# Kernel optimization log

Measured on AMD Instinct MI355X. Metric: run time of the kernel, lower is better.

## Reference

```python
import jax, jax.numpy as jnp
import numpy as np

N, CIN, H, W = 32, 128, 56, 56
COUT, KH, KW = 256, 3, 3
PH, PW, SH, SW = 1, 1, 1, 1


def setup_inputs() -> dict:
    key = jax.random.key(0)
    kx, kw_, kb = jax.random.split(key, 3)
    x = jax.random.normal(kx, (N, CIN, H, W), dtype=jnp.float32)
    # kaiming_normal_ fan_in, relu: std = sqrt(2 / fan_in)
    fan_in = CIN * KH * KW
    weight = jax.random.normal(kw_, (COUT, CIN, KH, KW), dtype=jnp.float32) * jnp.sqrt(2.0 / fan_in)
    bias = jnp.zeros((COUT,), dtype=jnp.float32)
    return {"x": x, "weight": weight, "bias": bias}


def reference(x, weight, bias):
    # NCHW input, OIHW weight -> NCHW output; zero padding, stride (SH, SW)
    y = jax.lax.conv_general_dilated(
        x, weight,
        window_strides=(SH, SW),
        padding=((PH, PH), (PW, PW)),
        dimension_numbers=("NCHW", "OIHW", "NCHW"),
    )
    return y + bias[None, :, None, None]
```

## Files before the change

### kernel.cpp

```cpp
#include <hip/hip_runtime.h>
#include <hip/hip_bf16.h>


typedef __attribute__((ext_vector_type(8))) short bf16x8;
typedef __attribute__((ext_vector_type(4))) float f32x4;
typedef __attribute__((ext_vector_type(8))) unsigned short u16x8;

#define AS1(p) ((const __attribute__((address_space(1))) unsigned int*)(p))
#define AS3(p) ((__attribute__((address_space(3))) unsigned int*)(p))
#define G_LDS16(g, l) __builtin_amdgcn_global_load_lds(AS1(g), AS3(l), 16, 0, 0)

#define XT_OFF (1u << 20)

__global__ __launch_bounds__(256) void k_wreorder(const float* __restrict__ w,
                                                  __hip_bfloat16* __restrict__ wt) {
    int t = blockIdx.x * 256 + threadIdx.x;
    if (t >= 9 * 256 * 128) return;
    int ci = t & 127;
    int co = (t >> 7) & 255;
    int khkw = t >> 15;
    wt[t] = __float2bfloat16(w[(co * 128 + ci) * 9 + khkw]);
}

__global__ __launch_bounds__(256) void k_xconv(const float* __restrict__ x,
                                               __hip_bfloat16* __restrict__ xt) {
    const int b = blockIdx.x;
    const int n = b / 58, ih = b % 58;
    __hip_bfloat16* row = xt + (size_t)b * 58 * 128;
    const int t = threadIdx.x;

    if (ih == 0 || ih == 57) {
        u16x8 z = {0, 0, 0, 0, 0, 0, 0, 0};
        for (int i = t; i < 928; i += 256)
            ((u16x8*)row)[i] = z;
        return;
    }

    const int h = ih - 1;
    __shared__ float tile[56][132];
    const float* xb = x + (size_t)n * 128 * 3136 + h * 56;
    for (int i = t; i < 1792; i += 256) {
        int ci = i / 14, w4 = i % 14;
        f32x4 v = *(const f32x4*)(xb + ci * 3136 + w4 * 4);
#pragma unroll
        for (int c = 0; c < 4; ++c)
            tile[w4 * 4 + c][ci] = v[c];
    }
    __syncthreads();

    if (t < 32) {
        u16x8 z = {0, 0, 0, 0, 0, 0, 0, 0};
        int iw = (t < 16) ? 0 : 57;
        ((u16x8*)(row + iw * 128))[t & 15] = z;
    }
    for (int i = t; i < 896; i += 256) {
        int p = i >> 4, g = i & 15;
        u16x8 o;
#pragma unroll
        for (int j = 0; j < 8; ++j) {
            __hip_bfloat16 bv = __float2bfloat16(tile[p][g * 8 + j]);
            o[j] = *reinterpret_cast<unsigned short*>(&bv);
        }
        *(u16x8*)((char*)row + (p + 1) * 256 + g * 16) = o;
    }
}

__global__ __launch_bounds__(512, 2) void k_conv_gemm(
    const __hip_bfloat16* __restrict__ wt,
    const __hip_bfloat16* __restrict__ xt,
    const float* __restrict__ bias,
    float* __restrict__ out)
{
    __shared__ char lds[256 * 128 + 128 * 128];
    char* ldsA = lds;
    char* ldsB = lds + 256 * 128;

    const int bid = blockIdx.x;
    const int blk = (bid & 7) * 98 + (bid >> 3);

    const int tid = threadIdx.x;
    const int lane = tid & 63, wave = tid >> 6;
    const int co_w = (wave >> 1) * 64;
    const int px_w = (wave & 1) * 64;

    const int lr = lane >> 3;
    const int lc = lane & 7;
    const int swz = ((lc ^ lr) << 4);

    unsigned int bsrc[2];
#pragma unroll
    for (int r = 0; r < 2; ++r) {
        int px = r * 64 + wave * 8 + lr;
        int p = blk * 128 + px;
        int n = p / 3136, rem = p - n * 3136;
        int oh = rem / 56, ow = rem - oh * 56;
        bsrc[r] = (unsigned)(((n * 58 + oh) * 58 + ow) * 256) + swz;
    }

    f32x4 acc[4][4] = {};

    for (int khkw = 0; khkw < 9; ++khkw) {
        const int kh = khkw / 3, kw = khkw - kh * 3;
        const unsigned koffB = (unsigned)((kh * 58 + kw) * 256);
        const unsigned aoff = (unsigned)(khkw * 65536);
        for (int ci2 = 0; ci2 < 256; ci2 += 128) {
#pragma unroll
            for (int r = 0; r < 4; ++r) {
                int co = r * 64 + wave * 8 + lr;
                G_LDS16((const char*)wt + aoff + ci2 + co * 256 + swz,
                        ldsA + (r * 64 + wave * 8) * 128);
            }
#pragma unroll
            for (int r = 0; r < 2; ++r) {
                G_LDS16((const char*)xt + bsrc[r] + koffB + ci2,
                        ldsB + (r * 64 + wave * 8) * 128);
            }
            __syncthreads();

#pragma unroll
            for (int ks = 0; ks < 2; ++ks) {
                bf16x8 af[4], bx[4];
#pragma unroll
                for (int m = 0; m < 4; ++m) {
                    int row = co_w + m * 16 + (lane & 15);
                    int koff = (ks * 64 + ((lane >> 4) * 16)) ^ ((row & 7) << 4);
                    af[m] = *(const bf16x8*)(ldsA + row * 128 + koff);
                }
#pragma unroll
                for (int nn = 0; nn < 4; ++nn) {
                    int row = px_w + nn * 16 + (lane & 15);
                    int koff = (ks * 64 + ((lane >> 4) * 16)) ^ ((row & 7) << 4);
                    bx[nn] = *(const bf16x8*)(ldsB + row * 128 + koff);
                }
#pragma unroll
                for (int m = 0; m < 4; ++m)
#pragma unroll
                    for (int nn = 0; nn < 4; ++nn)
                        acc[m][nn] = __builtin_amdgcn_mfma_f32_16x16x32_bf16(
                            af[m], bx[nn], acc[m][nn], 0, 0, 0);
            }
            __syncthreads();
        }
    }

    int obase[4];
#pragma unroll
    for (int nn = 0; nn < 4; ++nn) {
        int p = blk * 128 + px_w + nn * 16 + (lane & 15);
        int n = p / 3136, rem = p - n * 3136;
        obase[nn] = n * 802816 + rem;
    }
    const int rgrp = lane >> 4;
#pragma unroll
    for (int m = 0; m < 4; ++m) {
#pragma unroll
        for (int r = 0; r < 4; ++r) {
            int co = co_w + m * 16 + rgrp * 4 + r;
            float bv = bias[co];
#pragma unroll
            for (int nn = 0; nn < 4; ++nn)
                out[obase[nn] + co * 3136] = acc[m][nn][r] + bv;
        }
    }
}

extern "C" void kernel_launch(void* const* d_in, const int* in_sizes, int n_in,
                              void* d_out, int out_size, void* d_ws, size_t ws_size,
                              hipStream_t stream) {
    const float* x    = (const float*)d_in[0];
    const float* w    = (const float*)d_in[1];
    const float* bias = (const float*)d_in[2];
    float* out = (float*)d_out;

    char* ws = (char*)d_ws;
    __hip_bfloat16* wt = (__hip_bfloat16*)ws;
    __hip_bfloat16* xt = (__hip_bfloat16*)(ws + XT_OFF);

    k_wreorder<<<1152, 256, 0, stream>>>(w, wt);
    k_xconv<<<32 * 58, 256, 0, stream>>>(x, xt);
    k_conv_gemm<<<784, 512, 0, stream>>>(wt, xt, bias, out);
}
```

Baseline: 206.5 us.

## Double-buffer input tile in LDS and read weights directly from global

Stops staging the weight tile through LDS. Each wave now loads its A fragments straight from global memory (served by L1/L2). The input tile B is double-buffered in LDS so the next step's async load overlaps the current MFMA work, and only one barrier remains per step instead of two. This cuts LDS footprint and synchronization, but the weight reads now go to global memory in the inner loop without reuse across waves sharing rows, which may expose memory latency.

```diff
diff --git a/kernel.cpp b/kernel.cpp
--- a/kernel.cpp
+++ b/kernel.cpp
@@ -71,9 +71,7 @@
     const float* __restrict__ bias,
     float* __restrict__ out)
 {
-    __shared__ char lds[256 * 128 + 128 * 128];
-    char* ldsA = lds;
-    char* ldsB = lds + 256 * 128;
+    __shared__ char ldsB[2][128 * 128];
 
     const int bid = blockIdx.x;
     const int blk = (bid & 7) * 98 + (bid >> 3);
@@ -97,50 +95,55 @@
         bsrc[r] = (unsigned)(((n * 58 + oh) * 58 + ow) * 256) + swz;
     }
 
+    const unsigned abase = (unsigned)((co_w + (lane & 15)) * 256 + (lane >> 4) * 16);
+
     f32x4 acc[4][4] = {};
 
-    for (int khkw = 0; khkw < 9; ++khkw) {
-        const int kh = khkw / 3, kw = khkw - kh * 3;
-        const unsigned koffB = (unsigned)((kh * 58 + kw) * 256);
-        const unsigned aoff = (unsigned)(khkw * 65536);
-        for (int ci2 = 0; ci2 < 256; ci2 += 128) {
+    {
 #pragma unroll
-            for (int r = 0; r < 4; ++r) {
-                int co = r * 64 + wave * 8 + lr;
-                G_LDS16((const char*)wt + aoff + ci2 + co * 256 + swz,
-                        ldsA + (r * 64 + wave * 8) * 128);
+        for (int r = 0; r < 2; ++r)
+            G_LDS16((const char*)xt + bsrc[r] +  0 +  0,
+                    ldsB[0] + (r * 64 + wave * 8) * 128);
+    }
+    __syncthreads();
+
+    int cur = 0;
+    for (int step = 0; step < 18; ++step) {
+        if (step + 1 < 18) {
+            int s = step + 1;
+            int kk = s >> 1, cih = s & 1;
+            int kh = kk / 3, kw = kk - kh * 3;
+            unsigned off = (unsigned)((kh * 58 + kw) * 256 + cih * 128);
+#pragma unroll
+            for (int r = 0; r < 2; ++r)
+                G_LDS16((const char*)xt + bsrc[r] + off,
+                        ldsB[cur ^ 1] + (r * 64 + wave * 8) * 128);
+        }
+
+        const int kk = step >> 1, cih = step & 1;
+        const unsigned aoff = (unsigned)(kk * 65536 + cih * 128) + abase;
+
+#pragma unroll
+        for (int khalf = 0; khalf < 2; ++khalf) {
+            bf16x8 af[4], bx[4];
+#pragma unroll
+            for (int m = 0; m < 4; ++m)
+                af[m] = *(const bf16x8*)((const char*)wt + aoff + m * 4096 + khalf * 64);
+#pragma unroll
+            for (int nn = 0; nn < 4; ++nn) {
+                int row = px_w + nn * 16 + (lane & 15);
+                int koff = (khalf * 64 + ((lane >> 4) * 16)) ^ ((row & 7) << 4);
+                bx[nn] = *(const bf16x8*)(ldsB[cur] + row * 128 + koff);
             }
 #pragma unroll
-            for (int r = 0; r < 2; ++r) {
-                G_LDS16((const char*)xt + bsrc[r] + koffB + ci2,
-                        ldsB + (r * 64 + wave * 8) * 128);
-            }
-            __syncthreads();
-
+            for (int m = 0; m < 4; ++m)
 #pragma unroll
-            for (int ks = 0; ks < 2; ++ks) {
-                bf16x8 af[4], bx[4];
-#pragma unroll
-                for (int m = 0; m < 4; ++m) {
-                    int row = co_w + m * 16 + (lane & 15);
-                    int koff = (ks * 64 + ((lane >> 4) * 16)) ^ ((row & 7) << 4);
-                    af[m] = *(const bf16x8*)(ldsA + row * 128 + koff);
-                }
-#pragma unroll
-                for (int nn = 0; nn < 4; ++nn) {
-                    int row = px_w + nn * 16 + (lane & 15);
-                    int koff = (ks * 64 + ((lane >> 4) * 16)) ^ ((row & 7) << 4);
-                    bx[nn] = *(const bf16x8*)(ldsB + row * 128 + koff);
-                }
-#pragma unroll
-                for (int m = 0; m < 4; ++m)
-#pragma unroll
-                    for (int nn = 0; nn < 4; ++nn)
-                        acc[m][nn] = __builtin_amdgcn_mfma_f32_16x16x32_bf16(
-                            af[m], bx[nn], acc[m][nn], 0, 0, 0);
-            }
-            __syncthreads();
+                for (int nn = 0; nn < 4; ++nn)
+                    acc[m][nn] = __builtin_amdgcn_mfma_f32_16x16x32_bf16(
+                        af[m], bx[nn], acc[m][nn], 0, 0, 0);
         }
+        __syncthreads();
+        cur ^= 1;
     }
 
     int obase[4];
```

Result: slower. 285.2 us (+38.1%).

## Triple-buffer LDS stages with async prefetch and one barrier per step

Applied to the files above, without the earlier changes.

The conv GEMM main loop now uses three LDS slots. Global-to-LDS loads for step t+2 are issued while step t computes, and partial vmcnt waits replace the two __syncthreads per iteration with a single barrier. MFMA issue is wrapped in s_setprio to favour math waves. LDS use rises to 144 KB per block, which may prevent two blocks per CU from fitting as the launch bounds request, trading occupancy for latency hiding.

```diff
diff --git a/kernel.cpp b/kernel.cpp
--- a/kernel.cpp
+++ b/kernel.cpp
@@ -71,17 +71,15 @@
     const float* __restrict__ bias,
     float* __restrict__ out)
 {
-    __shared__ char lds[256 * 128 + 128 * 128];
-    char* ldsA = lds;
-    char* ldsB = lds + 256 * 128;
+    __shared__ char lds[3][384 * 128];
 
     const int bid = blockIdx.x;
     const int blk = (bid & 7) * 98 + (bid >> 3);
 
     const int tid = threadIdx.x;
     const int lane = tid & 63, wave = tid >> 6;
-    const int co_w = (wave >> 1) * 64;
-    const int px_w = (wave & 1) * 64;
+    const int wm = wave >> 1;
+    const int wn = wave & 1;
 
     const int lr = lane >> 3;
     const int lc = lane & 7;
@@ -97,56 +95,76 @@
         bsrc[r] = (unsigned)(((n * 58 + oh) * 58 + ow) * 256) + swz;
     }
 
+    auto stage = [&](int s, char* slot) {
+        const int kk = s >> 1, cih = s & 1;
+        const int kh = kk / 3, kw = kk - kh * 3;
+        const unsigned aoff = (unsigned)(kk * 65536 + cih * 128);
+#pragma unroll
+        for (int r = 0; r < 4; ++r) {
+            int row = r * 64 + wave * 8;
+            G_LDS16((const char*)wt + aoff + (row + lr) * 256 + swz,
+                    slot + row * 128);
+        }
+        const unsigned boff = (unsigned)((kh * 58 + kw) * 256 + cih * 128);
+#pragma unroll
+        for (int r = 0; r < 2; ++r) {
+            G_LDS16((const char*)xt + bsrc[r] + boff,
+                    slot + (256 + r * 64 + wave * 8) * 128);
+        }
+    };
+
     f32x4 acc[4][4] = {};
 
-    for (int khkw = 0; khkw < 9; ++khkw) {
-        const int kh = khkw / 3, kw = khkw - kh * 3;
-        const unsigned koffB = (unsigned)((kh * 58 + kw) * 256);
-        const unsigned aoff = (unsigned)(khkw * 65536);
-        for (int ci2 = 0; ci2 < 256; ci2 += 128) {
-#pragma unroll
-            for (int r = 0; r < 4; ++r) {
-                int co = r * 64 + wave * 8 + lr;
-                G_LDS16((const char*)wt + aoff + ci2 + co * 256 + swz,
-                        ldsA + (r * 64 + wave * 8) * 128);
+    stage(0, lds[0]);
+    stage(1, lds[1]);
+
+    char* cs = lds[0];
+    char* ns = lds[1];
+    char* ps = lds[2];
+
+    for (int t = 0; t < 18; ++t) {
+        if (t < 17) asm volatile("s_waitcnt vmcnt(6)" ::: "memory");
+        else        asm volatile("s_waitcnt vmcnt(0)" ::: "memory");
+        __builtin_amdgcn_s_barrier();
+        __builtin_amdgcn_sched_barrier(0);
+
+        if (t < 16) stage(t + 2, ps);
+
+        bf16x8 af[2][4], bx[2][4];
+#pragma unroll
+        for (int kh2 = 0; kh2 < 2; ++kh2) {
+#pragma unroll
+            for (int m = 0; m < 4; ++m) {
+                int row = wm * 64 + m * 16 + (lane & 15);
+                int koff = (kh2 * 64 + ((lane >> 4) * 16)) ^ ((row & 7) << 4);
+                af[kh2][m] = *(const bf16x8*)(cs + row * 128 + koff);
             }
 #pragma unroll
-            for (int r = 0; r < 2; ++r) {
-                G_LDS16((const char*)xt + bsrc[r] + koffB + ci2,
-                        ldsB + (r * 64 + wave * 8) * 128);
+            for (int nn = 0; nn < 4; ++nn) {
+                int row = wn * 64 + nn * 16 + (lane & 15);
+                int koff = (kh2 * 64 + ((lane >> 4) * 16)) ^ ((row & 7) << 4);
+                bx[kh2][nn] = *(const bf16x8*)(cs + (256 + row) * 128 + koff);
             }
-            __syncthreads();
-
-#pragma unroll
-            for (int ks = 0; ks < 2; ++ks) {
-                bf16x8 af[4], bx[4];
-#pragma unroll
-                for (int m = 0; m < 4; ++m) {
-                    int row = co_w + m * 16 + (lane & 15);
-                    int koff = (ks * 64 + ((lane >> 4) * 16)) ^ ((row & 7) << 4);
-                    af[m] = *(const bf16x8*)(ldsA + row * 128 + koff);
-                }
-#pragma unroll
-                for (int nn = 0; nn < 4; ++nn) {
-                    int row = px_w + nn * 16 + (lane & 15);
-                    int koff = (ks * 64 + ((lane >> 4) * 16)) ^ ((row & 7) << 4);
-                    bx[nn] = *(const bf16x8*)(ldsB + row * 128 + koff);
-                }
-#pragma unroll
-                for (int m = 0; m < 4; ++m)
-#pragma unroll
-                    for (int nn = 0; nn < 4; ++nn)
-                        acc[m][nn] = __builtin_amdgcn_mfma_f32_16x16x32_bf16(
-                            af[m], bx[nn], acc[m][nn], 0, 0, 0);
-            }
-            __syncthreads();
-        }
+        }
+
+        __builtin_amdgcn_s_setprio(1);
+#pragma unroll
+        for (int kh2 = 0; kh2 < 2; ++kh2)
+#pragma unroll
+            for (int m = 0; m < 4; ++m)
+#pragma unroll
+                for (int nn = 0; nn < 4; ++nn)
+                    acc[m][nn] = __builtin_amdgcn_mfma_f32_16x16x32_bf16(
+                        af[kh2][m], bx[kh2][nn], acc[m][nn], 0, 0, 0);
+        __builtin_amdgcn_s_setprio(0);
+
+        char* tmp = cs; cs = ns; ns = ps; ps = tmp;
     }
 
     int obase[4];
 #pragma unroll
     for (int nn = 0; nn < 4; ++nn) {
-        int p = blk * 128 + px_w + nn * 16 + (lane & 15);
+        int p = blk * 128 + wn * 64 + nn * 16 + (lane & 15);
         int n = p / 3136, rem = p - n * 3136;
         obase[nn] = n * 802816 + rem;
     }
@@ -155,7 +173,7 @@
     for (int m = 0; m < 4; ++m) {
 #pragma unroll
         for (int r = 0; r < 4; ++r) {
-            int co = co_w + m * 16 + rgrp * 4 + r;
+            int co = wm * 64 + m * 16 + rgrp * 4 + r;
             float bv = bias[co];
 #pragma unroll
             for (int nn = 0; nn < 4; ++nn)
```

Result: slower. 213.2 us (+3.2%).
